# Kernel tuning notes

Measured on AMD Instinct MI355X. Metric: run time of the kernel, lower is better.

The kernel has to match this reference:

```python
import jax, jax.numpy as jnp
import numpy as np


def conv2d(x, w, b, pad):
    out = jax.lax.conv_general_dilated(x, w, (1, 1), [(pad, pad), (pad, pad)],
                                       dimension_numbers=('NCHW', 'OIHW', 'NCHW'))
    if b is not None:
        out = out + b[None, :, None, None]
    return out


def propagate(x, conv1_w, conv1_b, res_ws, conv2_w, conv2_b):
    # conv_1 (k3,p1) -> ResidualStack -> relu -> conv_2 (k1)
    y = conv2d(x, conv1_w, conv1_b, 1)
    for w1, w2 in res_ws:
        h = conv2d(jax.nn.relu(y), w1, None, 1)   # 3x3, no bias
        h = conv2d(jax.nn.relu(h), w2, None, 0)   # 1x1, no bias
        y = y + h
    y = jax.nn.relu(y)
    return conv2d(y, conv2_w, conv2_b, 0)


def hopfield_q(y, patterns):
    # HopfieldLayer with static stored/state patterns: attention over learned pattern bank
    B, C, H, W = y.shape
    t = y.transpose(0, 2, 3, 1).reshape(B, H * W, C)                 # tokens [B,HW,C]
    logits = t @ patterns.T / jnp.sqrt(jnp.asarray(C, t.dtype))      # [B,HW,E]
    q = jax.nn.softmax(logits, axis=-1) @ patterns                   # [B,HW,C]
    return q.reshape(B, H, W, C).transpose(0, 3, 1, 2)


def setup_inputs() -> dict:
    key = jax.random.key(0)
    ks = jax.random.split(key, 10)
    B, Cin, Cout, H, RH, E = 8, 64, 32, 8, 32, 512
    s = 0.1  # keep the relu/conv stack numerically tame
    return {
        'x':        jax.random.normal(ks[0], (B, Cin, H, H), jnp.float32),
        'conv1_w':  s * jax.random.normal(ks[1], (Cin, Cin, 3, 3), jnp.float32),
        'conv1_b':  s * jax.random.normal(ks[2], (Cin,), jnp.float32),
        'res0_w1':  s * jax.random.normal(ks[3], (RH, Cin, 3, 3), jnp.float32),
        'res0_w2':  s * jax.random.normal(ks[4], (Cin, RH, 1, 1), jnp.float32),
        'res1_w1':  s * jax.random.normal(ks[5], (RH, Cin, 3, 3), jnp.float32),
        'res1_w2':  s * jax.random.normal(ks[6], (Cin, RH, 1, 1), jnp.float32),
        'conv2_w':  s * jax.random.normal(ks[7], (Cout, Cin, 1, 1), jnp.float32),
        'conv2_b':  s * jax.random.normal(ks[8], (Cout,), jnp.float32),
        'patterns': jax.random.normal(ks[9], (E, Cout), jnp.float32),
    }


def reference(x, conv1_w, conv1_b, res0_w1, res0_w2, res1_w1, res1_w2, conv2_w, conv2_b, patterns):
    res_ws = ((res0_w1, res0_w2), (res1_w1, res1_w2))
    B, Cin, H, W = x.shape
    Cout = conv2_w.shape[0]
    P = H * W  # square images: out_repres_dim == in_repres_dim == H

    def prop1(x1):  # per-sample propagate: [Cin,H,W] -> [Cout,H,W]
        return propagate(x1[None], conv1_w, conv1_b, res_ws, conv2_w, conv2_b)[0]

    def qerr1(x1):  # per-sample quantization error: [Cin,H,W] -> [H,W]
        y = prop1(x1)
        yq = jax.lax.stop_gradient(hopfield_q(y[None], patterns)[0])  # y_quant.detach()
        return ((y - yq) ** 2).sum(axis=0)

    # batch samples are independent, so per-sample jacobians == diagonal blocks used by torch
    e_jac = jax.vmap(jax.jacrev(qerr1))(x)    # [B,H,W,Cin,H,W]
    xy_jac = jax.vmap(jax.jacrev(prop1))(x)   # [B,Cout,H,W,Cin,H,W]

    e_total = e_jac.sum(axis=3).reshape(B, P, P)   # sum over Cin -> [B, out2, in2]
    idx = jnp.argmin(e_total, axis=1)              # [B, in2] routed output pixel per input pixel

    J = xy_jac.reshape(B, Cout, P, Cin, P)         # [B, Cout, out2, Cin, in2]
    x_flat = x.reshape(B, Cin, P)
    onehot = jax.nn.one_hot(idx, P, dtype=x.dtype)  # [B, in2, out2]
    # gather J at routed pixel m, contract x over Cin, scatter-add into m:
    # y_masked[b,o,m] = sum_i onehot[b,i,m] * sum_c x[b,c,i] * J[b,o,m,c,i]
    y_masked = jnp.einsum('bomci,bci,bim->bom', J, x_flat, onehot)

    return hopfield_q(y_masked.reshape(B, Cout, H, W), patterns)
```

## Files before the change

### kernel.cpp

```cpp
#include <hip/hip_runtime.h>
#include <math.h>


constexpr int OFF_MBIT = 0;
constexpr int OFF_N    = 3072;
constexpr int OFF_G    = OFF_N    + 32768;
constexpr int OFF_Y    = OFF_G    + 16384;
constexpr int OFF_X1W  = OFF_Y    + 16384;
constexpr int OFF_WSUM = OFF_X1W  + 294912;
constexpr int OFF_W1RT = OFF_WSUM + 640;
constexpr int OFF_W2RT = OFF_W1RT + 36864;
constexpr int OFF_WC2T = OFF_W2RT + 4096;
constexpr int OFF_W1T  = OFF_WC2T + 2048;
constexpr int OFF_T    = OFF_W1T  + 36864;
constexpr int OFF_IDX  = OFF_T    + 1048576;

__device__ __forceinline__ void conv3x3_tile(
    const float* __restrict__ Wg, const int COdim, const int co0,
    const float* __restrict__ Bp, const int ciBase, const int ciN,
    const int lr, const int lc, float acc[4][8])
{
#pragma unroll
  for (int k = 0; k < 9; k++) {
    const int dy = k / 3 - 1, dx = k % 3 - 1;
    const float* wrow = Wg + (k * 64 + ciBase) * COdim + co0 + lc * 4;
    const float* brow = Bp + ciBase * 80 + (1 + lr + dy) * 8;
#pragma unroll 4
    for (int ci = 0; ci < ciN; ci++) {
      float4 wv = *(const float4*)(wrow + ci * COdim);
      float4 b0 = *(const float4*)(brow + ci * 80);
      float4 b1 = *(const float4*)(brow + ci * 80 + 4);
      float bb[8] = {b0.x, b0.y, b0.z, b0.w, b1.x, b1.y, b1.z, b1.w};
      float wj[4] = {wv.x, wv.y, wv.z, wv.w};
#pragma unroll
      for (int j = 0; j < 4; j++)
#pragma unroll
        for (int px = 0; px < 8; px++) {
          const int sx = px + dx;
          if (sx >= 0 && sx <= 7) acc[j][px] = fmaf(wj[j], bb[sx], acc[j][px]);
        }
    }
  }
}

__device__ __forceinline__ void conv1x1_tile(
    const float* __restrict__ Wg, const int COdim, const int co0,
    const float* __restrict__ Bp, const int ciBase, const int ciN,
    const int lr, const int lc, float acc[4][8])
{
  const float* wbase = Wg + ciBase * COdim + co0 + lc * 4;
  const float* bbase = Bp + ciBase * 80 + (1 + lr) * 8;
#pragma unroll 4
  for (int ci = 0; ci < ciN; ci++) {
    float4 wv = *(const float4*)(wbase + ci * COdim);
    float4 b0 = *(const float4*)(bbase + ci * 80);
    float4 b1 = *(const float4*)(bbase + ci * 80 + 4);
    float bb[8] = {b0.x, b0.y, b0.z, b0.w, b1.x, b1.y, b1.z, b1.w};
    float wj[4] = {wv.x, wv.y, wv.z, wv.w};
#pragma unroll
    for (int j = 0; j < 4; j++)
#pragma unroll
      for (int px = 0; px < 8; px++)
        acc[j][px] = fmaf(wj[j], bb[px], acc[j][px]);
  }
}

__device__ __forceinline__ void conv1x1_flat(
    const float* __restrict__ Wg, const int COdim, const int co0,
    const float* __restrict__ Bf, const int ciBase, const int ciN,
    const int lr, const int lc, float acc[4][8])
{
  const float* wbase = Wg + ciBase * COdim + co0 + lc * 4;
  const float* bbase = Bf + ciBase * 64 + lr * 8;
#pragma unroll 4
  for (int ci = 0; ci < ciN; ci++) {
    float4 wv = *(const float4*)(wbase + ci * COdim);
    float4 b0 = *(const float4*)(bbase + ci * 64);
    float4 b1 = *(const float4*)(bbase + ci * 64 + 4);
    float bb[8] = {b0.x, b0.y, b0.z, b0.w, b1.x, b1.y, b1.z, b1.w};
    float wj[4] = {wv.x, wv.y, wv.z, wv.w};
#pragma unroll
    for (int j = 0; j < 4; j++)
#pragma unroll
      for (int px = 0; px < 8; px++)
        acc[j][px] = fmaf(wj[j], bb[px], acc[j][px]);
  }
}

__device__ __forceinline__ void store_tile(float* dst, int lr, int lc,
                                           const float acc[4][8])
{
#pragma unroll
  for (int j = 0; j < 4; j++) {
    *(float4*)(dst + (lc * 4 + j) * 64 + lr * 8) =
        make_float4(acc[j][0], acc[j][1], acc[j][2], acc[j][3]);
    *(float4*)(dst + (lc * 4 + j) * 64 + lr * 8 + 4) =
        make_float4(acc[j][4], acc[j][5], acc[j][6], acc[j][7]);
  }
}

__global__ __launch_bounds__(256) void kP(
    const float* __restrict__ x, const float* __restrict__ w1,
    const float* __restrict__ r0w1, const float* __restrict__ r0w2,
    const float* __restrict__ r1w1, const float* __restrict__ r1w2,
    const float* __restrict__ w2, float* ws)
{
  const int bk = blockIdx.x;
  const int t = threadIdx.x;
  __shared__ __align__(16) float Xp[5120];
  __shared__ __align__(16) float Pq[8192];
  __shared__ __align__(16) float Wk[4096];

  if (bk >= 72) {
    const int t0 = (bk - 72) * 256 + t;
    const int stride = 8 * 256;
    for (int e = t0; e < 18432; e += stride) {
      int co = e & 31, ci = (e >> 5) & 63, k = e >> 11;
      ws[OFF_W1RT + e]         = r0w1[(co * 64 + ci) * 9 + k];
      ws[OFF_W1RT + 18432 + e] = r1w1[(co * 64 + ci) * 9 + k];
    }
    for (int e = t0; e < 2048; e += stride) {
      int co = e & 63, ci = e >> 6;
      ws[OFF_W2RT + e]        = r0w2[co * 32 + ci];
      ws[OFF_W2RT + 2048 + e] = r1w2[co * 32 + ci];
      int o = e & 31, c2 = e >> 5;
      ws[OFF_WC2T + e] = w2[o * 64 + c2];
    }
    for (int e = t0; e < 576; e += stride) {
      int k = e >> 6, co = e & 63;
      float a = 0.f;
      for (int ci = 0; ci < 64; ci++) a += w1[(co * 64 + ci) * 9 + k];
      ws[OFF_WSUM + e] = a;
    }
    return;
  }

  const int b = bk / 9, k = bk % 9;
  const int w = t >> 6, lane = t & 63;
  const int lr = lane >> 3, lc = lane & 7;
  for (int e = t; e < 4096; e += 256) {
    int ci = e >> 6, p = e & 63;
    Xp[ci * 80 + 8 + p] = x[b * 4096 + e];
  }
  for (int e = t; e < 4096; e += 256) {
    int ci = e >> 6, co = e & 63;
    Wk[e] = w1[(co * 64 + ci) * 9 + k];
  }
  __syncthreads();
  float acc[4][8];
#pragma unroll
  for (int j = 0; j < 4; j++)
#pragma unroll
    for (int px = 0; px < 8; px++) acc[j][px] = 0.f;
  const int cohalf = w & 1, ks = w >> 1;
  conv1x1_tile(Wk, 64, cohalf * 32, Xp, ks * 32, 32, lr, lc, acc);
  store_tile(Pq + ks * 4096 + cohalf * 2048, lr, lc, acc);
  __syncthreads();
  for (int e = t; e < 4096; e += 256) {
    int co = e & 63, i = e >> 6;
    int pin = (co >> 5) * 2048 + (co & 31) * 64 + i;
    ws[OFF_X1W + ((b * 64 + i) * 9 + k) * 64 + co] = Pq[pin] + Pq[4096 + pin];
  }
}

__global__ __launch_bounds__(1024) void kF(
    const float* __restrict__ b1, const float* __restrict__ b2,
    const float* __restrict__ wsc, float* ws)
{
  const int b = blockIdx.x, t = threadIdx.x;
  const int w = t >> 6, lane = t & 63, lr = lane >> 3, lc = lane & 7;
  __shared__ __align__(16) float Apad[5120];
  __shared__ __align__(16) float Yl[4096];
  __shared__ __align__(16) float Pq[18432];
  __shared__ __align__(16) float Hpad[2560];
  __shared__ __align__(16) float Wsm[2048];
  __shared__ __align__(16) float Wsm2[2048];
  unsigned int* wsi = (unsigned int*)ws;

  if (t < 1024) {
    int ci = t >> 4, r9 = (t >> 3) & 1, c = t & 7;
    Apad[ci * 80 + r9 * 72 + c] = 0.f;
  }
  if (t < 512) {
    int ci = t >> 4, r9 = (t >> 3) & 1, c = t & 7;
    Hpad[ci * 80 + r9 * 72 + c] = 0.f;
  }

  {
    const int co4 = t & 15, p = t >> 4;
    const int py = p >> 3, px = p & 7;
    float4 a = ((const float4*)b1)[co4];
#pragma unroll
    for (int k = 0; k < 9; k++) {
      int dy = k / 3 - 1, dx = k % 3 - 1;
      int qy = py + dy, qx = px + dx;
      if ((unsigned)qy < 8u && (unsigned)qx < 8u) {
        int ik = qy * 8 + qx;
        float4 v = *(const float4*)(wsc + OFF_X1W + ((b * 64 + ik) * 9 + k) * 64 + co4 * 4);
        a.x += v.x; a.y += v.y; a.z += v.z; a.w += v.w;
      }
    }
    float av[4] = {a.x, a.y, a.z, a.w};
#pragma unroll
    for (int j = 0; j < 4; j++) {
      int co = co4 * 4 + j;
      Yl[co * 64 + p] = av[j];
      Apad[co * 80 + 8 + p] = fmaxf(av[j], 0.f);
    }
  }
  __syncthreads();
  if (t < 64) {
    unsigned int lo = 0, hi = 0;
#pragma unroll
    for (int ci = 0; ci < 32; ci++) lo |= (Yl[ci * 64 + t] > 0.f ? 1u : 0u) << ci;
#pragma unroll
    for (int ci = 0; ci < 32; ci++) hi |= (Yl[(32 + ci) * 64 + t] > 0.f ? 1u : 0u) << ci;
    wsi[OFF_MBIT + ((b * 3 + 0) * 64 + t) * 2]     = lo;
    wsi[OFF_MBIT + ((b * 3 + 0) * 64 + t) * 2 + 1] = hi;
  }

  float acc[4][8];
  for (int s = 0; s < 2; s++) {
    {
      const float2* src = (const float2*)(wsc + OFF_W1RT + s * 18432);
      float2* dst = (float2*)Pq;
#pragma unroll
      for (int z = 0; z < 9; z++) dst[z * 1024 + t] = src[z * 1024 + t];
    }
    __syncthreads();
    if (w < 8) {
#pragma unroll
      for (int j = 0; j < 4; j++)
#pragma unroll
        for (int px = 0; px < 8; px++) acc[j][px] = 0.f;
      conv3x3_tile(Pq, 32, 0, Apad, w * 8, 8, lr, lc, acc);
    } else {
      int tt = t - 512;
#pragma unroll
      for (int z = 0; z < 4; z++) Wsm[z * 512 + tt] = wsc[OFF_W2RT + s * 2048 + z * 512 + tt];
      if (s == 1) {
#pragma unroll
        for (int z = 0; z < 4; z++) Wsm2[z * 512 + tt] = wsc[OFF_WC2T + z * 512 + tt];
      }
    }
    __syncthreads();
    if (w < 8) store_tile(Pq + w * 2048, lr, lc, acc);
    __syncthreads();
    for (int e = t; e < 2048; e += 1024) {
      int rh = e >> 6, p = e & 63;
      float hv = 0.f;
#pragma unroll
      for (int ks = 0; ks < 8; ks++) hv += Pq[ks * 2048 + e];
      ws[OFF_N + (b * 2 + s) * 2048 + e] = hv > 0.f ? 1.f : 0.f;
      Hpad[rh * 80 + 8 + p] = fmaxf(hv, 0.f);
    }
    __syncthreads();
    if (w < 8) {
#pragma unroll
      for (int j = 0; j < 4; j++)
#pragma unroll
        for (int px = 0; px < 8; px++) acc[j][px] = 0.f;
      const int cohalf = w & 1, ks = w >> 1;
      conv1x1_tile(Wsm, 64, cohalf * 32, Hpad, ks * 8, 8, lr, lc, acc);
      store_tile(Pq + ks * 4096 + cohalf * 2048, lr, lc, acc);
    }
    __syncthreads();
    for (int e = t; e < 4096; e += 1024) {
      int co = e >> 6, p = e & 63;
      int pin = (co >> 5) * 2048 + (co & 31) * 64 + p;
      float d = 0.f;
#pragma unroll
      for (int ks = 0; ks < 4; ks++) d += Pq[ks * 4096 + pin];
      float ny = Yl[e] + d;
      Yl[e] = ny;
      Apad[co * 80 + 8 + p] = fmaxf(ny, 0.f);
    }
    __syncthreads();
    if (t < 64) {
      unsigned int lo = 0, hi = 0;
#pragma unroll
      for (int ci = 0; ci < 32; ci++) lo |= (Yl[ci * 64 + t] > 0.f ? 1u : 0u) << ci;
#pragma unroll
      for (int ci = 0; ci < 32; ci++) hi |= (Yl[(32 + ci) * 64 + t] > 0.f ? 1u : 0u) << ci;
      wsi[OFF_MBIT + ((b * 3 + 1 + s) * 64 + t) * 2]     = lo;
      wsi[OFF_MBIT + ((b * 3 + 1 + s) * 64 + t) * 2 + 1] = hi;
    }
  }

  if (w < 8) {
#pragma unroll
    for (int j = 0; j < 4; j++)
#pragma unroll
      for (int px = 0; px < 8; px++) acc[j][px] = 0.f;
    conv1x1_tile(Wsm2, 32, 0, Apad, w * 8, 8, lr, lc, acc);
    store_tile(Pq + w * 2048, lr, lc, acc);
  }
  __syncthreads();
  for (int e = t; e < 2048; e += 1024) {
    int o = e >> 6, p = e & 63;
    float yv = b2[o];
#pragma unroll
    for (int ks = 0; ks < 8; ks++) yv += Pq[ks * 2048 + e];
    ws[OFF_Y + b * 2048 + p * 32 + o] = yv;
  }
}

__global__ __launch_bounds__(64) void kHopG(const float* __restrict__ wsc,
                                            const float* __restrict__ pat,
                                            float* __restrict__ ws)
{
  const int b = blockIdx.x >> 6, tok = blockIdx.x & 63;
  const int lane = threadIdx.x;
  const float* yp = wsc + OFF_Y + b * 2048 + tok * 32;
  float4 ya[8];
#pragma unroll
  for (int r = 0; r < 8; r++) ya[r] = ((const float4*)yp)[r];

  float l[8];
#pragma unroll
  for (int j = 0; j < 8; j++) {
    const float4* pp = (const float4*)(pat + (j * 64 + lane) * 32);
    float lj = 0.f;
#pragma unroll
    for (int c4 = 0; c4 < 8; c4++) {
      float4 pv = pp[c4];
      lj = fmaf(ya[c4].x, pv.x, lj);
      lj = fmaf(ya[c4].y, pv.y, lj);
      lj = fmaf(ya[c4].z, pv.z, lj);
      lj = fmaf(ya[c4].w, pv.w, lj);
    }
    l[j] = lj * 0.17677669529663687f;
  }
  float mx = -1e30f;
#pragma unroll
  for (int j = 0; j < 8; j++) mx = fmaxf(mx, l[j]);
#pragma unroll
  for (int off = 32; off > 0; off >>= 1) mx = fmaxf(mx, __shfl_xor(mx, off, 64));
  float num[8]; float dsum = 0.f;
#pragma unroll
  for (int j = 0; j < 8; j++) { num[j] = __expf(l[j] - mx); dsum += num[j]; }
#pragma unroll
  for (int off = 32; off > 0; off >>= 1) dsum += __shfl_xor(dsum, off, 64);

  float q[32];
#pragma unroll
  for (int c = 0; c < 32; c++) q[c] = 0.f;
#pragma unroll
  for (int j = 0; j < 8; j++) {
    const float4* pp = (const float4*)(pat + (j * 64 + lane) * 32);
    float nj = num[j];
#pragma unroll
    for (int c4 = 0; c4 < 8; c4++) {
      float4 pv = pp[c4];
      q[c4 * 4 + 0] = fmaf(nj, pv.x, q[c4 * 4 + 0]);
      q[c4 * 4 + 1] = fmaf(nj, pv.y, q[c4 * 4 + 1]);
      q[c4 * 4 + 2] = fmaf(nj, pv.z, q[c4 * 4 + 2]);
      q[c4 * 4 + 3] = fmaf(nj, pv.w, q[c4 * 4 + 3]);
    }
  }
#pragma unroll
  for (int off = 32; off > 0; off >>= 1) {
#pragma unroll
    for (int c = 0; c < 32; c++) q[c] += __shfl_xor(q[c], off, 64);
  }
  if (lane == 0) {
    float invd = 1.f / dsum;
    float yy[32];
#pragma unroll
    for (int c4 = 0; c4 < 8; c4++) {
      yy[c4 * 4 + 0] = ya[c4].x; yy[c4 * 4 + 1] = ya[c4].y;
      yy[c4 * 4 + 2] = ya[c4].z; yy[c4 * 4 + 3] = ya[c4].w;
    }
    float* gp = ws + OFF_G + b * 2048 + tok * 32;
#pragma unroll
    for (int c4 = 0; c4 < 8; c4++)
      *(float4*)(gp + c4 * 4) = make_float4(
          2.f * (yy[c4 * 4 + 0] - q[c4 * 4 + 0] * invd),
          2.f * (yy[c4 * 4 + 1] - q[c4 * 4 + 1] * invd),
          2.f * (yy[c4 * 4 + 2] - q[c4 * 4 + 2] * invd),
          2.f * (yy[c4 * 4 + 3] - q[c4 * 4 + 3] * invd));
  }
}

__global__ __launch_bounds__(128) void kJ(const float* __restrict__ wsc, float* ws)
{
  const int bid = blockIdx.x;
  const int type = bid & 1, i = (bid >> 1) & 63, b = bid >> 7;
  const int t = threadIdx.x;
  const int w = t >> 6, p = t & 63;
  const int lr = p >> 3, lc = p & 7;
  const int py = p >> 3, px = p & 7, iy = i >> 3, ix = i & 7;
  __shared__ __align__(16) float Up[5120];
  __shared__ __align__(16) float Pp[4096];
  const unsigned int* wsi = (const unsigned int*)wsc;

  float Tch[32];
  {
    int kh = iy - py + 1, kw = ix - px + 1;
    bool v0 = (unsigned)kh < 3u && (unsigned)kw < 3u;
    int kidx = v0 ? kh * 3 + kw : 0;
    const float4* s4 = (const float4*)(type
        ? (wsc + OFF_X1W + ((b * 64 + i) * 9 + kidx) * 64)
        : (wsc + OFF_WSUM + kidx * 64)) + w * 8;
#pragma unroll
    for (int c4 = 0; c4 < 8; c4++) {
      float4 tv = s4[c4];
      Tch[c4 * 4 + 0] = v0 ? tv.x : 0.f;
      Tch[c4 * 4 + 1] = v0 ? tv.y : 0.f;
      Tch[c4 * 4 + 2] = v0 ? tv.z : 0.f;
      Tch[c4 * 4 + 3] = v0 ? tv.w : 0.f;
    }
  }

  float accA[4][8];
  for (int s = 0; s < 2; s++) {
    if (s) __syncthreads();
    unsigned int mw = wsi[OFF_MBIT + ((b * 3 + s) * 64 + p) * 2 + w];
#pragma unroll
    for (int c = 0; c < 32; c++)
      Up[(w * 32 + c) * 80 + 8 + p] = ((mw >> c) & 1u) ? Tch[c] : 0.f;
#pragma unroll
    for (int z = 0; z < 8; z++) {
      int e = z * 64 + p;
      int ci = w * 32 + (e >> 4);
      Up[ci * 80 + ((e >> 3) & 1) * 72 + (e & 7)] = 0.f;
    }
#pragma unroll
    for (int j = 0; j < 4; j++)
#pragma unroll
      for (int pq = 0; pq < 8; pq++) accA[j][pq] = 0.f;
    conv3x3_tile(wsc + OFF_W1RT + s * 18432, 32, 0, Up, w * 32, 32, lr, lc, accA);
    store_tile(Pp + w * 2048, lr, lc, accA);
    __syncthreads();
    {
      float4* Pp4 = (float4*)Pp;
      const float4* Np4 = (const float4*)(wsc + OFF_N + (b * 2 + s) * 2048);
#pragma unroll
      for (int z = 0; z < 4; z++) {
        int e4 = z * 128 + t;
        float4 a = Pp4[e4], bq = Pp4[512 + e4], nv = Np4[e4];
        Pp4[e4] = make_float4((a.x + bq.x) * nv.x, (a.y + bq.y) * nv.y,
                              (a.z + bq.z) * nv.z, (a.w + bq.w) * nv.w);
      }
    }
    __syncthreads();
#pragma unroll
    for (int j = 0; j < 4; j++)
#pragma unroll
      for (int pq = 0; pq < 8; pq++) accA[j][pq] = 0.f;
    conv1x1_flat(wsc + OFF_W2RT + s * 2048, 64, w * 32, Pp, 0, 32, lr, lc, accA);
    store_tile(Up + w * 2048, lr, lc, accA);
#pragma unroll
    for (int c = 0; c < 32; c++) Tch[c] += Up[w * 2048 + c * 64 + p];
  }
  __syncthreads();
  {
    unsigned int mw = wsi[OFF_MBIT + ((b * 3 + 2) * 64 + p) * 2 + w];
#pragma unroll
    for (int c = 0; c < 32; c++)
      Up[(w * 32 + c) * 64 + p] = ((mw >> c) & 1u) ? Tch[c] : 0.f;
#pragma unroll
    for (int j = 0; j < 4; j++)
#pragma unroll
      for (int pq = 0; pq < 8; pq++) accA[j][pq] = 0.f;
    conv1x1_flat(wsc + OFF_WC2T, 32, 0, Up, w * 32, 32, lr, lc, accA);
    store_tile(Pp + w * 2048, lr, lc, accA);
  }
  __syncthreads();

  if (type == 0) {
    if (w == 0) {
      const float* gp = wsc + OFF_G + b * 2048 + p * 32;
      float e = 0.f;
#pragma unroll
      for (int o4 = 0; o4 < 8; o4++) {
        float4 gv = *(const float4*)(gp + o4 * 4);
        int o = o4 * 4;
        e = fmaf(gv.x, Pp[(o + 0) * 64 + p] + Pp[2048 + (o + 0) * 64 + p], e);
        e = fmaf(gv.y, Pp[(o + 1) * 64 + p] + Pp[2048 + (o + 1) * 64 + p], e);
        e = fmaf(gv.z, Pp[(o + 2) * 64 + p] + Pp[2048 + (o + 2) * 64 + p], e);
        e = fmaf(gv.w, Pp[(o + 3) * 64 + p] + Pp[2048 + (o + 3) * 64 + p], e);
      }
      float bv = e; int bi = p;
#pragma unroll
      for (int off = 1; off < 64; off <<= 1) {
        float ov = __shfl_xor(bv, off, 64);
        int oi = __shfl_xor(bi, off, 64);
        if (ov < bv || (ov == bv && oi < bi)) { bv = ov; bi = oi; }
      }
      if (p == 0) ((int*)(ws + OFF_IDX))[b * 64 + i] = bi;
    }
  } else {
    float* Tp = ws + OFF_T + (b * 64 + i) * 2048;
#pragma unroll
    for (int z = 0; z < 4; z++) {
      int e4 = z * 128 + t;
      int m = e4 >> 3, o0 = (e4 & 7) * 4;
      *(float4*)(Tp + e4 * 4) = make_float4(
          Pp[(o0 + 0) * 64 + m] + Pp[2048 + (o0 + 0) * 64 + m],
          Pp[(o0 + 1) * 64 + m] + Pp[2048 + (o0 + 1) * 64 + m],
          Pp[(o0 + 2) * 64 + m] + Pp[2048 + (o0 + 2) * 64 + m],
          Pp[(o0 + 3) * 64 + m] + Pp[2048 + (o0 + 3) * 64 + m]);
    }
  }
}

__global__ __launch_bounds__(64) void kQ(const float* __restrict__ wsc,
                                         const float* __restrict__ pat,
                                         float* __restrict__ outp)
{
  const int b = blockIdx.x >> 6, tok = blockIdx.x & 63;
  const int lane = threadIdx.x;
  const int sidx = ((const int*)(wsc + OFF_IDX))[b * 64 + lane];
  const bool sel = (sidx == tok);
  float ym[32];
  const float4* Tp = (const float4*)(wsc + OFF_T + ((b * 64 + lane) * 64 + tok) * 32);
#pragma unroll
  for (int c4 = 0; c4 < 8; c4++) {
    float4 tv = Tp[c4];
    ym[c4 * 4 + 0] = sel ? tv.x : 0.f;
    ym[c4 * 4 + 1] = sel ? tv.y : 0.f;
    ym[c4 * 4 + 2] = sel ? tv.z : 0.f;
    ym[c4 * 4 + 3] = sel ? tv.w : 0.f;
  }
#pragma unroll
  for (int off = 1; off < 64; off <<= 1) {
#pragma unroll
    for (int c = 0; c < 32; c++) ym[c] += __shfl_xor(ym[c], off, 64);
  }
  float l[8];
#pragma unroll
  for (int j = 0; j < 8; j++) {
    const float4* pp = (const float4*)(pat + (j * 64 + lane) * 32);
    float lj = 0.f;
#pragma unroll
    for (int c4 = 0; c4 < 8; c4++) {
      float4 pv = pp[c4];
      lj = fmaf(ym[c4 * 4 + 0], pv.x, lj);
      lj = fmaf(ym[c4 * 4 + 1], pv.y, lj);
      lj = fmaf(ym[c4 * 4 + 2], pv.z, lj);
      lj = fmaf(ym[c4 * 4 + 3], pv.w, lj);
    }
    l[j] = lj * 0.17677669529663687f;
  }
  float mx = -1e30f;
#pragma unroll
  for (int j = 0; j < 8; j++) mx = fmaxf(mx, l[j]);
#pragma unroll
  for (int off = 32; off > 0; off >>= 1) mx = fmaxf(mx, __shfl_xor(mx, off, 64));
  float num[8]; float dsum = 0.f;
#pragma unroll
  for (int j = 0; j < 8; j++) { num[j] = __expf(l[j] - mx); dsum += num[j]; }
#pragma unroll
  for (int off = 32; off > 0; off >>= 1) dsum += __shfl_xor(dsum, off, 64);
  float q[32];
#pragma unroll
  for (int c = 0; c < 32; c++) q[c] = 0.f;
#pragma unroll
  for (int j = 0; j < 8; j++) {
    const float4* pp = (const float4*)(pat + (j * 64 + lane) * 32);
    float nj = num[j];
#pragma unroll
    for (int c4 = 0; c4 < 8; c4++) {
      float4 pv = pp[c4];
      q[c4 * 4 + 0] = fmaf(nj, pv.x, q[c4 * 4 + 0]);
      q[c4 * 4 + 1] = fmaf(nj, pv.y, q[c4 * 4 + 1]);
      q[c4 * 4 + 2] = fmaf(nj, pv.z, q[c4 * 4 + 2]);
      q[c4 * 4 + 3] = fmaf(nj, pv.w, q[c4 * 4 + 3]);
    }
  }
#pragma unroll
  for (int off = 32; off > 0; off >>= 1) {
#pragma unroll
    for (int c = 0; c < 32; c++) q[c] += __shfl_xor(q[c], off, 64);
  }
  if (lane == 0) {
    float invd = 1.f / dsum;
#pragma unroll
    for (int c = 0; c < 32; c++)
      outp[b * 2048 + c * 64 + tok] = q[c] * invd;
  }
}

extern "C" void kernel_launch(void* const* d_in, const int* in_sizes, int n_in,
                              void* d_out, int out_size, void* d_ws, size_t ws_size,
                              hipStream_t stream) {
  (void)in_sizes; (void)n_in; (void)out_size; (void)ws_size;
  const float* x    = (const float*)d_in[0];
  const float* w1   = (const float*)d_in[1];
  const float* b1   = (const float*)d_in[2];
  const float* r0w1 = (const float*)d_in[3];
  const float* r0w2 = (const float*)d_in[4];
  const float* r1w1 = (const float*)d_in[5];
  const float* r1w2 = (const float*)d_in[6];
  const float* w2   = (const float*)d_in[7];
  const float* b2   = (const float*)d_in[8];
  const float* pat  = (const float*)d_in[9];
  float* ws  = (float*)d_ws;
  float* out = (float*)d_out;

  kP<<<80, 256, 0, stream>>>(x, w1, r0w1, r0w2, r1w1, r1w2, w2, ws);
  kF<<<8, 1024, 0, stream>>>(b1, b2, ws, ws);
  kHopG<<<512, 64, 0, stream>>>(ws, pat, ws);
  kJ<<<1024, 128, 0, stream>>>(ws, ws);
  kQ<<<512, 64, 0, stream>>>(ws, pat, out);
}
```

Baseline: 231.1 us.

## Split kJ input channels across four waves with LDS atomic reduction

kJ now runs with 256 threads (four wavefronts) instead of 128. Each wave handles 16 input channels of the 3x3 conv, and the partial results are reduced into a padded shared buffer with LDS atomicAdd instead of a stored-then-summed pair of tiles. The 1x1 convs are re-tiled so each thread produces fewer output channels, and padded strides (68) are used to reduce bank conflicts. The aim is more parallelism per block and less per-thread serial work and register pressure, at the cost of extra barriers, LDS atomics and a changed float summation order.

```diff
diff --git a/kernel.cpp b/kernel.cpp
--- a/kernel.cpp
+++ b/kernel.cpp
@@ -65,28 +65,6 @@
   }
 }
 
-__device__ __forceinline__ void conv1x1_flat(
-    const float* __restrict__ Wg, const int COdim, const int co0,
-    const float* __restrict__ Bf, const int ciBase, const int ciN,
-    const int lr, const int lc, float acc[4][8])
-{
-  const float* wbase = Wg + ciBase * COdim + co0 + lc * 4;
-  const float* bbase = Bf + ciBase * 64 + lr * 8;
-#pragma unroll 4
-  for (int ci = 0; ci < ciN; ci++) {
-    float4 wv = *(const float4*)(wbase + ci * COdim);
-    float4 b0 = *(const float4*)(bbase + ci * 64);
-    float4 b1 = *(const float4*)(bbase + ci * 64 + 4);
-    float bb[8] = {b0.x, b0.y, b0.z, b0.w, b1.x, b1.y, b1.z, b1.w};
-    float wj[4] = {wv.x, wv.y, wv.z, wv.w};
-#pragma unroll
-    for (int j = 0; j < 4; j++)
-#pragma unroll
-      for (int px = 0; px < 8; px++)
-        acc[j][px] = fmaf(wj[j], bb[px], acc[j][px]);
-  }
-}
-
 __device__ __forceinline__ void store_tile(float* dst, int lr, int lc,
                                            const float acc[4][8])
 {
@@ -382,7 +360,7 @@
   }
 }
 
-__global__ __launch_bounds__(128) void kJ(const float* __restrict__ wsc, float* ws)
+__global__ __launch_bounds__(256, 4) void kJ(const float* __restrict__ wsc, float* ws)
 {
   const int bid = blockIdx.x;
   const int type = bid & 1, i = (bid >> 1) & 63, b = bid >> 7;
@@ -391,80 +369,132 @@
   const int lr = p >> 3, lc = p & 7;
   const int py = p >> 3, px = p & 7, iy = i >> 3, ix = i & 7;
   __shared__ __align__(16) float Up[5120];
-  __shared__ __align__(16) float Pp[4096];
+  __shared__ __align__(16) float Vf[2176];
   const unsigned int* wsi = (const unsigned int*)wsc;
 
-  float Tch[32];
+  float Tq[16];
   {
     int kh = iy - py + 1, kw = ix - px + 1;
     bool v0 = (unsigned)kh < 3u && (unsigned)kw < 3u;
     int kidx = v0 ? kh * 3 + kw : 0;
     const float4* s4 = (const float4*)(type
         ? (wsc + OFF_X1W + ((b * 64 + i) * 9 + kidx) * 64)
-        : (wsc + OFF_WSUM + kidx * 64)) + w * 8;
-#pragma unroll
-    for (int c4 = 0; c4 < 8; c4++) {
+        : (wsc + OFF_WSUM + kidx * 64)) + w * 4;
+#pragma unroll
+    for (int c4 = 0; c4 < 4; c4++) {
       float4 tv = s4[c4];
-      Tch[c4 * 4 + 0] = v0 ? tv.x : 0.f;
-      Tch[c4 * 4 + 1] = v0 ? tv.y : 0.f;
-      Tch[c4 * 4 + 2] = v0 ? tv.z : 0.f;
-      Tch[c4 * 4 + 3] = v0 ? tv.w : 0.f;
-    }
-  }
-
-  float accA[4][8];
+      Tq[c4 * 4 + 0] = v0 ? tv.x : 0.f;
+      Tq[c4 * 4 + 1] = v0 ? tv.y : 0.f;
+      Tq[c4 * 4 + 2] = v0 ? tv.z : 0.f;
+      Tq[c4 * 4 + 3] = v0 ? tv.w : 0.f;
+    }
+  }
+
+  float acc[4][8];
   for (int s = 0; s < 2; s++) {
     if (s) __syncthreads();
-    unsigned int mw = wsi[OFF_MBIT + ((b * 3 + s) * 64 + p) * 2 + w];
-#pragma unroll
-    for (int c = 0; c < 32; c++)
-      Up[(w * 32 + c) * 80 + 8 + p] = ((mw >> c) & 1u) ? Tch[c] : 0.f;
-#pragma unroll
-    for (int z = 0; z < 8; z++) {
-      int e = z * 64 + p;
-      int ci = w * 32 + (e >> 4);
-      Up[ci * 80 + ((e >> 3) & 1) * 72 + (e & 7)] = 0.f;
-    }
+    for (int e = p; e < 544; e += 64) Vf[w * 544 + e] = 0.f;
+    {
+      unsigned int mword = wsi[OFF_MBIT + ((b * 3 + s) * 64 + p) * 2 + (w >> 1)];
+      unsigned int mq = (mword >> ((w & 1) * 16)) & 0xFFFFu;
+#pragma unroll
+      for (int c = 0; c < 16; c++)
+        Up[(16 * w + c) * 80 + 8 + p] = ((mq >> c) & 1u) ? Tq[c] : 0.f;
+#pragma unroll
+      for (int z = 0; z < 4; z++) {
+        int e = z * 64 + p;
+        int ci = 16 * w + (e >> 4);
+        Up[ci * 80 + ((e >> 3) & 1) * 72 + (e & 7)] = 0.f;
+      }
+    }
+    __syncthreads();
 #pragma unroll
     for (int j = 0; j < 4; j++)
 #pragma unroll
-      for (int pq = 0; pq < 8; pq++) accA[j][pq] = 0.f;
-    conv3x3_tile(wsc + OFF_W1RT + s * 18432, 32, 0, Up, w * 32, 32, lr, lc, accA);
-    store_tile(Pp + w * 2048, lr, lc, accA);
-    __syncthreads();
+      for (int pq = 0; pq < 8; pq++) acc[j][pq] = 0.f;
+    conv3x3_tile(wsc + OFF_W1RT + s * 18432, 32, 0, Up, w * 16, 16, lr, lc, acc);
     {
-      float4* Pp4 = (float4*)Pp;
-      const float4* Np4 = (const float4*)(wsc + OFF_N + (b * 2 + s) * 2048);
-#pragma unroll
-      for (int z = 0; z < 4; z++) {
-        int e4 = z * 128 + t;
-        float4 a = Pp4[e4], bq = Pp4[512 + e4], nv = Np4[e4];
-        Pp4[e4] = make_float4((a.x + bq.x) * nv.x, (a.y + bq.y) * nv.y,
-                              (a.z + bq.z) * nv.z, (a.w + bq.w) * nv.w);
-      }
-    }
-    __syncthreads();
-#pragma unroll
-    for (int j = 0; j < 4; j++)
-#pragma unroll
-      for (int pq = 0; pq < 8; pq++) accA[j][pq] = 0.f;
-    conv1x1_flat(wsc + OFF_W2RT + s * 2048, 64, w * 32, Pp, 0, 32, lr, lc, accA);
-    store_tile(Up + w * 2048, lr, lc, accA);
-#pragma unroll
-    for (int c = 0; c < 32; c++) Tch[c] += Up[w * 2048 + c * 64 + p];
+      const float* Np = wsc + OFF_N + (b * 2 + s) * 2048;
+#pragma unroll
+      for (int j = 0; j < 4; j++) {
+        int rh = lc * 4 + j;
+        float4 n0 = *(const float4*)(Np + rh * 64 + lr * 8);
+        float4 n1 = *(const float4*)(Np + rh * 64 + lr * 8 + 4);
+        float* vrow = &Vf[rh * 68 + lr * 8];
+        atomicAdd(vrow + 0, acc[j][0] * n0.x);
+        atomicAdd(vrow + 1, acc[j][1] * n0.y);
+        atomicAdd(vrow + 2, acc[j][2] * n0.z);
+        atomicAdd(vrow + 3, acc[j][3] * n0.w);
+        atomicAdd(vrow + 4, acc[j][4] * n1.x);
+        atomicAdd(vrow + 5, acc[j][5] * n1.y);
+        atomicAdd(vrow + 6, acc[j][6] * n1.z);
+        atomicAdd(vrow + 7, acc[j][7] * n1.w);
+      }
+    }
+    __syncthreads();
+    {
+      float a2[2][8];
+#pragma unroll
+      for (int j = 0; j < 2; j++)
+#pragma unroll
+        for (int pq = 0; pq < 8; pq++) a2[j][pq] = 0.f;
+      const float* wbase = wsc + OFF_W2RT + s * 2048 + 16 * w + lc * 2;
+      const float* bbase = Vf + lr * 8;
+#pragma unroll 4
+      for (int ci = 0; ci < 32; ci++) {
+        float2 wv = *(const float2*)(wbase + ci * 64);
+        float4 b0 = *(const float4*)(bbase + ci * 68);
+        float4 b1 = *(const float4*)(bbase + ci * 68 + 4);
+        float bb[8] = {b0.x, b0.y, b0.z, b0.w, b1.x, b1.y, b1.z, b1.w};
+#pragma unroll
+        for (int pq = 0; pq < 8; pq++) {
+          a2[0][pq] = fmaf(wv.x, bb[pq], a2[0][pq]);
+          a2[1][pq] = fmaf(wv.y, bb[pq], a2[1][pq]);
+        }
+      }
+#pragma unroll
+      for (int j = 0; j < 2; j++) {
+        int co = 16 * w + lc * 2 + j;
+        *(float4*)(&Up[co * 68 + lr * 8]) =
+            make_float4(a2[j][0], a2[j][1], a2[j][2], a2[j][3]);
+        *(float4*)(&Up[co * 68 + lr * 8 + 4]) =
+            make_float4(a2[j][4], a2[j][5], a2[j][6], a2[j][7]);
+      }
+#pragma unroll
+      for (int c = 0; c < 16; c++) Tq[c] += Up[(16 * w + c) * 68 + p];
+    }
   }
   __syncthreads();
   {
-    unsigned int mw = wsi[OFF_MBIT + ((b * 3 + 2) * 64 + p) * 2 + w];
-#pragma unroll
-    for (int c = 0; c < 32; c++)
-      Up[(w * 32 + c) * 64 + p] = ((mw >> c) & 1u) ? Tch[c] : 0.f;
-#pragma unroll
-    for (int j = 0; j < 4; j++)
-#pragma unroll
-      for (int pq = 0; pq < 8; pq++) accA[j][pq] = 0.f;
-    conv1x1_flat(wsc + OFF_WC2T, 32, 0, Up, w * 32, 32, lr, lc, accA);
-    store_tile(Pp + w * 2048, lr, lc, accA);
+    unsigned int mword = wsi[OFF_MBIT + ((b * 3 + 2) * 64 + p) * 2 + (w >> 1)];
+    unsigned int mq = (mword >> ((w & 1) * 16)) & 0xFFFFu;
+#pragma unroll
+    for (int c = 0; c < 16; c++)
+      Up[(16 * w + c) * 68 + p] = ((mq >> c) & 1u) ? Tq[c] : 0.f;
+  }
+  __syncthreads();
+  {
+    float a1[8];
+#pragma unroll
+    for (int pq = 0; pq < 8; pq++) a1[pq] = 0.f;
+    const float* wc = wsc + OFF_WC2T + 8 * w + lc;
+    const float* bbase = Up + lr * 8;
+#pragma unroll 4
+    for (int ci = 0; ci < 64; ci++) {
+      float wv = wc[ci * 32];
+      float4 b0 = *(const float4*)(bbase + ci * 68);
+      float4 b1 = *(const float4*)(bbase + ci * 68 + 4);
+      a1[0] = fmaf(wv, b0.x, a1[0]);
+      a1[1] = fmaf(wv, b0.y, a1[1]);
+      a1[2] = fmaf(wv, b0.z, a1[2]);
+      a1[3] = fmaf(wv, b0.w, a1[3]);
+      a1[4] = fmaf(wv, b1.x, a1[4]);
+      a1[5] = fmaf(wv, b1.y, a1[5]);
+      a1[6] = fmaf(wv, b1.z, a1[6]);
+      a1[7] = fmaf(wv, b1.w, a1[7]);
+    }
+    *(float4*)(&Vf[(8 * w + lc) * 68 + lr * 8]) = make_float4(a1[0], a1[1], a1[2], a1[3]);
+    *(float4*)(&Vf[(8 * w + lc) * 68 + lr * 8 + 4]) = make_float4(a1[4], a1[5], a1[6], a1[7]);
   }
   __syncthreads();
 
@@ -476,10 +506,10 @@
       for (int o4 = 0; o4 < 8; o4++) {
         float4 gv = *(const float4*)(gp + o4 * 4);
         int o = o4 * 4;
-        e = fmaf(gv.x, Pp[(o + 0) * 64 + p] + Pp[2048 + (o + 0) * 64 + p], e);
-        e = fmaf(gv.y, Pp[(o + 1) * 64 + p] + Pp[2048 + (o + 1) * 64 + p], e);
-        e = fmaf(gv.z, Pp[(o + 2) * 64 + p] + Pp[2048 + (o + 2) * 64 + p], e);
-        e = fmaf(gv.w, Pp[(o + 3) * 64 + p] + Pp[2048 + (o + 3) * 64 + p], e);
+        e = fmaf(gv.x, Vf[(o + 0) * 68 + p], e);
+        e = fmaf(gv.y, Vf[(o + 1) * 68 + p], e);
+        e = fmaf(gv.z, Vf[(o + 2) * 68 + p], e);
+        e = fmaf(gv.w, Vf[(o + 3) * 68 + p], e);
       }
       float bv = e; int bi = p;
 #pragma unroll
@@ -493,14 +523,12 @@
   } else {
     float* Tp = ws + OFF_T + (b * 64 + i) * 2048;
 #pragma unroll
-    for (int z = 0; z < 4; z++) {
-      int e4 = z * 128 + t;
+    for (int z = 0; z < 2; z++) {
+      int e4 = z * 256 + t;
       int m = e4 >> 3, o0 = (e4 & 7) * 4;
       *(float4*)(Tp + e4 * 4) = make_float4(
-          Pp[(o0 + 0) * 64 + m] + Pp[2048 + (o0 + 0) * 64 + m],
-          Pp[(o0 + 1) * 64 + m] + Pp[2048 + (o0 + 1) * 64 + m],
-          Pp[(o0 + 2) * 64 + m] + Pp[2048 + (o0 + 2) * 64 + m],
-          Pp[(o0 + 3) * 64 + m] + Pp[2048 + (o0 + 3) * 64 + m]);
+          Vf[(o0 + 0) * 68 + m], Vf[(o0 + 1) * 68 + m],
+          Vf[(o0 + 2) * 68 + m], Vf[(o0 + 3) * 68 + m]);
     }
   }
 }
@@ -602,6 +630,6 @@
   kP<<<80, 256, 0, stream>>>(x, w1, r0w1, r0w2, r1w1, r1w2, w2, ws);
   kF<<<8, 1024, 0, stream>>>(b1, b2, ws, ws);
   kHopG<<<512, 64, 0, stream>>>(ws, pat, ws);
-  kJ<<<1024, 128, 0, stream>>>(ws, ws);
+  kJ<<<1024, 256, 0, stream>>>(ws, ws);
   kQ<<<512, 64, 0, stream>>>(ws, pat, out);
 }
```

New measurement: 322.2 us. 1.39x slower.
